# Performance work log

Measured on AMD Instinct MI355X. Metric: run time of the kernel, lower is better.

## Reference

```python
import jax, jax.numpy as jnp
import numpy as np

N = 32; AUD = 128; MO = 256; LXM = 128; L = 600; B = 20; BL = 30
AH = 256; AE = 256; HID = 1024; OUT = 256; DEPTH = 2
IN_DIM = MO + AE + LXM      # 640
GRU_IN = IN_DIM + HID       # 1664


def gelu(x):
    return jax.nn.gelu(x, approximate=False)


def conv1d(x, w, b, stride=1, pad=0):
    y = jax.lax.conv_general_dilated(x, w, (stride,), [(pad, pad)],
                                     dimension_numbers=('NCH', 'OIH', 'NCH'))
    return y + b[None, :, None]


def layernorm(x, g, b, eps=1e-5):
    mu = jnp.mean(x, -1, keepdims=True)
    var = jnp.mean((x - mu) ** 2, -1, keepdims=True)
    return (x - mu) * jax.lax.rsqrt(var + eps) * g + b


def gru_cell(x, h, wih, whh, bih, bhh):
    gi = x @ wih.T + bih
    gh = h @ whh.T + bhh
    ir, iz, inn = jnp.split(gi, 3, -1)
    hr, hz, hn = jnp.split(gh, 3, -1)
    r = jax.nn.sigmoid(ir + hr)
    z = jax.nn.sigmoid(iz + hz)
    n = jnp.tanh(inn + r * hn)
    return (1.0 - z) * n + z * h


def setup_inputs():
    key = jax.random.key(0)
    ks = jax.random.split(key, 32)
    rn = lambda i, sh: jax.random.normal(ks[i], sh, jnp.float32) * 0.02
    z = lambda d: jnp.zeros((d,), jnp.float32)
    return {
        'aud': jax.random.normal(ks[0], (N, AUD, L), jnp.float32),
        'mo': jax.random.normal(ks[1], (N, MO, L), jnp.float32),
        'lxm': jax.random.normal(ks[2], (N, LXM, B), jnp.float32),
        'ae_w0': rn(3, (AH, AUD, 7)), 'ae_b0': z(AH),
        'ae_w1': rn(4, (AH, AH, 5)), 'ae_b1': z(AH),
        'ae_w2': rn(5, (AE, AH, 4)), 'ae_b2': z(AE),
        'ae_w3': rn(6, (AE, AE)), 'ae_b3': z(AE),
        'ae_ln_g': jnp.ones((AE,), jnp.float32), 'ae_ln_b': z(AE),
        'ci_w0': rn(7, (HID, MO + LXM)), 'ci_b0': z(HID),
        'ci_w1': rn(8, (HID, HID)), 'ci_b1': z(HID),
        'ci_w2': rn(9, (HID * DEPTH, HID)), 'ci_b2': z(HID * DEPTH),
        'dec_in_w': rn(10, (HID, IN_DIM)), 'dec_in_b': z(HID),
        'gru_wih0': rn(11, (3 * HID, GRU_IN)), 'gru_whh0': rn(12, (3 * HID, HID)),
        'gru_bih0': z(3 * HID), 'gru_bhh0': z(3 * HID),
        'gru_wih1': rn(13, (3 * HID, HID)), 'gru_whh1': rn(14, (3 * HID, HID)),
        'gru_bih1': z(3 * HID), 'gru_bhh1': z(3 * HID),
        'dec_ln_g': jnp.ones((HID,), jnp.float32), 'dec_ln_b': z(HID),
        'pred_w': rn(15, (OUT, HID)), 'pred_b': z(OUT),
    }


def reference(aud, mo, lxm, ae_w0, ae_b0, ae_w1, ae_b1, ae_w2, ae_b2, ae_w3, ae_b3,
              ae_ln_g, ae_ln_b, ci_w0, ci_b0, ci_w1, ci_b1, ci_w2, ci_b2,
              dec_in_w, dec_in_b, gru_wih0, gru_whh0, gru_bih0, gru_bhh0,
              gru_wih1, gru_whh1, gru_bih1, gru_bhh1, dec_ln_g, dec_ln_b,
              pred_w, pred_b):
    Nb = B - 2
    # Overlapping 3*BL audio windows for all blocks, encoded in one batched pass.
    win = jnp.stack([aud[:, :, b * BL:(b + 3) * BL] for b in range(Nb)], 0)  # [Nb,N,AUD,3BL]
    x = win.reshape(Nb * N, AUD, 3 * BL)
    x = gelu(conv1d(x, ae_w0, ae_b0))
    x = gelu(conv1d(x, ae_w1, ae_b1))
    x = gelu(conv1d(x, ae_w2, ae_b2, stride=2, pad=1))
    x = jnp.transpose(x, (0, 2, 1))                  # NDL -> NLD
    x = gelu(x @ ae_w3.T + ae_b3)
    x = layernorm(x, ae_ln_g, ae_ln_b)
    # Only frames 0..BL-1 of each encoded window are consumed by the decode loop.
    aud_seq = jnp.transpose(x[:, :BL, :].reshape(Nb, N, BL, AE), (0, 2, 1, 3)).reshape(Nb * BL, N, AE)
    lxm_seq = jnp.repeat(jnp.transpose(lxm[:, :, 1:B - 1], (2, 0, 1)), BL, axis=0)  # [T,N,LXM]
    # Cell state initializer.
    ci = gelu(jnp.concatenate([mo[:, :, BL - 1], lxm[:, :, 0]], -1) @ ci_w0.T + ci_b0)
    ci = gelu(ci @ ci_w1.T + ci_b1)
    h0 = jnp.transpose((ci @ ci_w2.T + ci_b2).reshape(N, DEPTH, HID), (1, 0, 2))  # [DEPTH,N,HID]

    def step(carry, inputs):
        pre_mo, h = carry
        a_t, l_t = inputs
        xcat = jnp.concatenate([pre_mo, a_t, l_t], -1)
        emb = gelu(xcat @ dec_in_w.T + dec_in_b)
        gin = jnp.concatenate([emb, xcat], -1)
        h0n = gru_cell(gin, h[0], gru_wih0, gru_whh0, gru_bih0, gru_bhh0)
        h1n = gru_cell(h0n, h[1], gru_wih1, gru_whh1, gru_bih1, gru_bhh1)
        pred = layernorm(h1n, dec_ln_g, dec_ln_b) @ pred_w.T + pred_b
        return (pred, jnp.stack([h0n, h1n])), pred

    _, preds = jax.lax.scan(step, (mo[:, :, BL - 1], h0), (aud_seq, lxm_seq))
    return jnp.transpose(preds, (1, 2, 0))  # [N, OUT, (B-2)*BL]
```

## Files before the change

kernel.cpp:

```cpp
#include <hip/hip_runtime.h>


typedef unsigned short u16;
typedef __attribute__((ext_vector_type(8))) short short8;
typedef __attribute__((ext_vector_type(4))) float f32x4;

#define GELU_FLG 1
#define BF16_FLG 2
#define NBLK 213
#define DEC_STEPS 540

__device__ __forceinline__ u16 f2b(float f){
  union { float f; unsigned u; } c; c.f = f;
  return (u16)((c.u + 0x7fffu + ((c.u >> 16) & 1u)) >> 16);
}
__device__ __forceinline__ short8 ld8(const u16* p){
  return *reinterpret_cast<const short8*>(p);
}
__device__ __forceinline__ short8 lds8(const void* p){
  return *reinterpret_cast<const short8*>(p);
}
__device__ __forceinline__ float ldfc(const float* p){
  return __hip_atomic_load(p, __ATOMIC_RELAXED, __HIP_MEMORY_SCOPE_AGENT);
}
__device__ __forceinline__ void stfc(float* p, float v){
  __hip_atomic_store(p, v, __ATOMIC_RELAXED, __HIP_MEMORY_SCOPE_AGENT);
}
__device__ __forceinline__ void stu32c(void* p, unsigned v){
  __hip_atomic_store((unsigned*)p, v, __ATOMIC_RELAXED, __HIP_MEMORY_SCOPE_AGENT);
}
__device__ __forceinline__ void st16c(u16* p, unsigned v){
  asm volatile("global_store_short %0, %1, off sc0 sc1" :: "v"(p), "v"(v) : "memory");
}
__device__ __forceinline__ f32x4 mfma16(short8 a, short8 b, f32x4 c){
  return __builtin_amdgcn_mfma_f32_16x16x32_bf16(a, b, c, 0, 0, 0);
}
__device__ __forceinline__ float gelu_f(float x){
  return 0.5f * x * (1.f + erff(x * 0.70710678118654752f));
}
__device__ __forceinline__ float sigmoid_f(float x){
  return 1.f / (1.f + __expf(-x));
}
__device__ __forceinline__ float tanh_f(float x){
  float e = __expf(-2.f * x);
  return (1.f - e) / (1.f + e);
}

template<int KB>
__device__ __forceinline__ void stageN(unsigned* ldsbase, const void* gbase, int lane, int q){
  const char* g = (const char*)gbase;
  #pragma unroll
  for (int c = 0; c < KB / 4; ++c){
    int cc = q + c * 4;
    __builtin_amdgcn_global_load_lds((const unsigned*)(g + (size_t)cc * 1024 + lane * 16),
                                     ldsbase + cc * 256, 16, 0, 0);
  }
}


__global__ void f2b_k(const float* __restrict__ s, u16* __restrict__ d, int n){
  int i = blockIdx.x * 256 + threadIdx.x;
  if (i < n) d[i] = f2b(s[i]);
}

__global__ void gather_xc_k(const float* __restrict__ mo, const float* __restrict__ lxm,
                            u16* __restrict__ xc, u16* __restrict__ pre_mo){
  int i = blockIdx.x * 256 + threadIdx.x;
  if (i >= 32 * 384) return;
  int n = i / 384, c = i - n * 384;
  float v = (c < 256) ? mo[(size_t)(n * 256 + c) * 600 + 29]
                      : lxm[(size_t)(n * 128 + (c - 256)) * 20];
  u16 h = f2b(v);
  xc[i] = h;
  if (c < 256) pre_mo[n * 256 + c] = h;
}

__global__ void lxm_g_k(const float* __restrict__ lxm, u16* __restrict__ o){
  int i = blockIdx.x * 256 + threadIdx.x;
  if (i >= 18 * 32 * 128) return;
  int c = i & 127, rest = i >> 7;
  int n = rest & 31, b = rest >> 5;
  o[i] = f2b(lxm[(size_t)(n * 128 + c) * 20 + 1 + b]);
}

__global__ void split_h_k(const float* __restrict__ hraw, u16* __restrict__ h0, u16* __restrict__ h1,
                          float* __restrict__ h0f, float* __restrict__ h1f){
  int i = blockIdx.x * 256 + threadIdx.x;
  if (i >= 32 * 1024) return;
  int n = i >> 10, c = i & 1023;
  float a = hraw[(size_t)n * 2048 + c];
  float b = hraw[(size_t)n * 2048 + 1024 + c];
  h0[i] = f2b(a); h1[i] = f2b(b);
  h0f[i] = a;     h1f[i] = b;
}

__global__ void build_xc0_k(const u16* __restrict__ pre_mo, const u16* __restrict__ aud_seq,
                            const u16* __restrict__ lxm_b, u16* __restrict__ xc0){
  int i = blockIdx.x * 256 + threadIdx.x;
  if (i >= 32 * 640) return;
  int n = i / 640, c = i - n * 640;
  u16 v;
  if (c < 256) v = pre_mo[n * 256 + c];
  else if (c < 512) v = aud_seq[n * 256 + (c - 256)];
  else v = lxm_b[n * 128 + (c - 512)];
  xc0[i] = v;
}

__global__ void swz_emb_k(const u16* __restrict__ src, u16* __restrict__ dst){
  int i = blockIdx.x * 256 + threadIdx.x;
  if (i >= 32 * 1024) return;
  int row = i >> 10, col = i & 1023;
  unsigned boff = (unsigned)(row * 2048) + (((unsigned)col * 2) ^ ((row & 7) << 4));
  *(u16*)((char*)dst + boff) = src[i];
}

__global__ void t_wpT_k(const float* __restrict__ wp, u16* __restrict__ wpT){
  int i = blockIdx.x * 256 + threadIdx.x;
  if (i >= 1024 * 256) return;
  int h = i >> 8, j = i & 255;
  wpT[i] = f2b(wp[(size_t)j * 1024 + h]);
}

__global__ void foldW_k(const float* __restrict__ src, const float* __restrict__ g,
                        const float* __restrict__ b, const float* __restrict__ addb,
                        u16* __restrict__ Wg, float* __restrict__ S, float* __restrict__ B, int R){
  int row = blockIdx.x * 4 + (threadIdx.x >> 6);
  if (row >= R) return;
  int lane = threadIdx.x & 63;
  const float* sr = src + (size_t)row * 1024;
  float s = 0.f, bb = 0.f;
  #pragma unroll
  for (int k = 0; k < 16; ++k){
    int c = lane + k * 64;
    float w = sr[c], gw = w * g[c];
    Wg[(size_t)row * 1024 + c] = f2b(gw);
    s += gw; bb += w * b[c];
  }
  #pragma unroll
  for (int m = 1; m < 64; m <<= 1){ s += __shfl_xor(s, m); bb += __shfl_xor(bb, m); }
  if (lane == 0){ S[row] = s; B[row] = bb + (addb ? addb[row] : 0.f); }
}

__global__ void vfold_k(const float* __restrict__ W, int ldw, int off, const float* __restrict__ pb,
                        const float* __restrict__ base, float* __restrict__ v, int R){
  int row = blockIdx.x * 4 + (threadIdx.x >> 6);
  if (row >= R) return;
  int lane = threadIdx.x & 63;
  const float* wr = W + (size_t)row * ldw + off;
  float s = 0.f;
  #pragma unroll
  for (int k = 0; k < 4; ++k){ int j = lane + k * 64; s += wr[j] * pb[j]; }
  #pragma unroll
  for (int m = 1; m < 64; m <<= 1) s += __shfl_xor(s, m);
  if (lane == 0) v[row] = s + (base ? base[row] : 0.f);
}


__global__ void im2col0_k(const float* __restrict__ aud, u16* __restrict__ A, int row0, long long tot){
  long long i = (long long)blockIdx.x * 256 + threadIdx.x;
  if (i >= tot) return;
  int k = (int)(i % 896);
  int row = row0 + (int)(i / 896);
  int ci = k / 7, kk = k - ci * 7;
  int p = row % 84, bn = row / 84;
  int b = bn >> 5, n = bn & 31;
  A[i] = f2b(aud[(size_t)(n * 128 + ci) * 600 + b * 30 + p + kk]);
}

__global__ void im2col1_k(const u16* __restrict__ O0, u16* __restrict__ A, int row0, long long tot){
  long long i = (long long)blockIdx.x * 256 + threadIdx.x;
  if (i >= tot) return;
  int k = (int)(i % 1280);
  int row = row0 + (int)(i / 1280);
  int ci = k / 5, kk = k - ci * 5;
  int p = row % 80, bn = row / 80;
  A[i] = O0[(size_t)(bn * 84 + p + kk) * 256 + ci];
}

__global__ void im2col2_k(const u16* __restrict__ O1, u16* __restrict__ A, int row0, long long tot){
  long long i = (long long)blockIdx.x * 256 + threadIdx.x;
  if (i >= tot) return;
  int k = (int)(i & 1023);
  int row = row0 + (int)(i >> 10);
  int ci = k >> 2, kk = k & 3;
  int p = row % 40, bn = row / 40;
  int pos = 2 * p - 1 + kk;
  A[i] = (pos >= 0 && pos < 80) ? O1[(size_t)(bn * 80 + pos) * 256 + ci] : (u16)0;
}


__global__ void gemm_bt(const u16* __restrict__ A, int lda,
                        const u16* __restrict__ W, int ldw, const float* __restrict__ bias,
                        void* __restrict__ outp, int M, int N, int K, int flags){
  const int lane = threadIdx.x & 63, widx = threadIdx.x >> 6;
  const int m0 = blockIdx.x * 64 + widx * 16;
  if (m0 >= M) return;
  const int n0 = blockIdx.y * 64;
  const int r = lane & 15, g4 = lane >> 4;
  const u16* arow = A + (size_t)(m0 + r) * lda + g4 * 8;
  const u16* wrow = W + (size_t)(n0 + r) * ldw + g4 * 8;
  f32x4 acc[4];
  const f32x4 FZ = {0.f, 0.f, 0.f, 0.f};
  acc[0] = FZ; acc[1] = FZ; acc[2] = FZ; acc[3] = FZ;
  for (int k = 0; k < K; k += 32){
    short8 a = ld8(arow + k);
    #pragma unroll
    for (int j = 0; j < 4; ++j)
      acc[j] = mfma16(a, ld8(wrow + (size_t)j * 16 * ldw + k), acc[j]);
  }
  #pragma unroll
  for (int j = 0; j < 4; ++j){
    int col = n0 + j * 16 + r;
    float bv = bias ? bias[col] : 0.f;
    #pragma unroll
    for (int q = 0; q < 4; ++q){
      int row = m0 + g4 * 4 + q;
      float v = acc[j][q] + bv;
      if (flags & GELU_FLG) v = gelu_f(v);
      if (flags & BF16_FLG) ((u16*)outp)[(size_t)row * N + col] = f2b(v);
      else                  ((float*)outp)[(size_t)row * N + col] = v;
    }
  }
}


__global__ void enc_ln_k(const float* __restrict__ O3, const float* __restrict__ g,
                         const float* __restrict__ bb, u16* __restrict__ aud_seq){
  int rid = blockIdx.x * 4 + (threadIdx.x >> 6);
  int lane = threadIdx.x & 63;
  int b = rid / 960, rem = rid - b * 960;
  int p2 = rem >> 5, n = rem & 31;
  int orow = (b * 32 + n) * 40 + p2;
  const float4 v = *reinterpret_cast<const float4*>(O3 + (size_t)orow * 256 + lane * 4);
  float s  = v.x + v.y + v.z + v.w;
  float s2 = v.x * v.x + v.y * v.y + v.z * v.z + v.w * v.w;
  #pragma unroll
  for (int m = 1; m < 64; m <<= 1){ s += __shfl_xor(s, m); s2 += __shfl_xor(s2, m); }
  float mu = s * (1.f / 256.f);
  float var = s2 * (1.f / 256.f) - mu * mu;
  float rs = rsqrtf(var + 1e-5f);
  int c = lane * 4;
  u16* dst = aud_seq + (size_t)rid * 256 + c;
  dst[0] = f2b((v.x - mu) * rs * g[c + 0] + bb[c + 0]);
  dst[1] = f2b((v.y - mu) * rs * g[c + 1] + bb[c + 1]);
  dst[2] = f2b((v.z - mu) * rs * g[c + 2] + bb[c + 2]);
  dst[3] = f2b((v.w - mu) * rs * g[c + 3] + bb[c + 3]);
}


struct DecArgs {
  const u16 *aud_seq, *lxm_b;
  const u16 *wih0, *whh0, *wih1, *whh1, *wd;
  const u16 *wpg, *Wdpg, *Wgpg;
  const float *Sp, *Bp, *S1, *B1, *S2, *B2, *vX, *vG;
  const float *bih0, *bhh0, *bih1, *bhh1;
  const u16 *h0init, *h1init;
  u16 *embR, *h0R, *h1R;
  float *statsR;
  float *GxR, *XalR, *GalR;
  float *h0f, *h1f, *out;
  int *sync;
};

__device__ __forceinline__ void sigslot(int* slot, int ep){
  asm volatile("s_waitcnt vmcnt(0)" ::: "memory");
  __syncthreads();
  if (threadIdx.x == 0)
    __hip_atomic_store(slot, ep, __ATOMIC_RELAXED, __HIP_MEMORY_SCOPE_AGENT);
}
__device__ __forceinline__ void waitflag(const int* flag, int tgt){
  if (threadIdx.x == 0){
    while (__hip_atomic_load(flag, __ATOMIC_RELAXED, __HIP_MEMORY_SCOPE_AGENT) < tgt)
      __builtin_amdgcn_s_sleep(1);
  }
  __syncthreads();
}
__device__ __forceinline__ void stage_fence(){
  asm volatile("s_waitcnt vmcnt(0)" ::: "memory");
  __syncthreads();
}

__global__ __launch_bounds__(256, 1) void decode_k(DecArgs A){
  const int tid = threadIdx.x;
  const int lane = tid & 63, q = tid >> 6;
  const int r = lane & 15, g4 = lane >> 4;
  const int blk = blockIdx.x;
  __shared__ __align__(16) unsigned smw[25088];
  char* const stg = (char*)smw;
  float* const exch = (float*)(smw + 16384);
  float* const stgStats = (float*)(smw + 16384);
  const f32x4 FZ = {0.f, 0.f, 0.f, 0.f};
  const int sw = (r & 7) << 4;
  int* const slotH0 = A.sync;
  int* const slotH1 = A.sync + 128 * 16;
  int* const slotPE = A.sync + 256 * 16;
  int* const slotAL = A.sync + 384 * 16;
  int* const flagH0 = A.sync + 512 * 16;
  int* const flagH1 = A.sync + 768 * 16;
  int* const flagPE = A.sync + 1024 * 16;
  int* const flagAL = A.sync + 1280 * 16;

  if (blk < 64){
    const int c0 = blk * 16;
    const int kq = q * 256;
    int* const myFpe = flagPE + blk * 16;
    int* const myFh0 = flagH0 + blk * 16;
    int* const mySlot = slotH0 + blk * 16;
    short8 we[24], wh[24];
    #pragma unroll
    for (int g = 0; g < 3; ++g)
      #pragma unroll
      for (int ch = 0; ch < 8; ++ch){
        we[g * 8 + ch] = ld8(A.wih0 + (size_t)(g * 1024 + c0 + r) * 1664 + kq + ch * 32 + g4 * 8);
        wh[g * 8 + ch] = ld8(A.whh0 + (size_t)(g * 1024 + c0 + r) * 1024 + kq + ch * 32 + g4 * 8);
      }
    const int n_c = tid >> 3;
    const int cc0 = (tid & 7) * 2;
    const int colA = c0 + cc0, colB = colA + 1;
    const unsigned stoff = (unsigned)(n_c * 2048) + (((unsigned)colA * 2) ^ ((n_c & 7) << 4));
    const float bi_r[2] = {A.bih0[colA], A.bih0[colB]};
    const float bi_z[2] = {A.bih0[1024 + colA], A.bih0[1024 + colB]};
    const float bi_n[2] = {A.bih0[2048 + colA], A.bih0[2048 + colB]};
    const float bh_r[2] = {A.bhh0[colA], A.bhh0[colB]};
    const float bh_z[2] = {A.bhh0[1024 + colA], A.bhh0[1024 + colB]};
    const float bh_n[2] = {A.bhh0[2048 + colA], A.bhh0[2048 + colB]};
    f32x4 ar[2], az[2], ani[2], anh[2];
    ar[0] = FZ; ar[1] = FZ; az[0] = FZ; az[1] = FZ; ani[0] = FZ; ani[1] = FZ; anh[0] = FZ; anh[1] = FZ;
    #pragma unroll
    for (int ch = 0; ch < 8; ++ch){
      short8 a0 = ld8(A.h0init + r * 1024 + kq + ch * 32 + g4 * 8);
      short8 a1 = ld8(A.h0init + (16 + r) * 1024 + kq + ch * 32 + g4 * 8);
      ar[0] = mfma16(a0, wh[ch], ar[0]);        ar[1] = mfma16(a1, wh[ch], ar[1]);
      az[0] = mfma16(a0, wh[8 + ch], az[0]);    az[1] = mfma16(a1, wh[8 + ch], az[1]);
      anh[0] = mfma16(a0, wh[16 + ch], anh[0]); anh[1] = mfma16(a1, wh[16 + ch], anh[1]);
    }
    #pragma unroll 1
    for (int t = 0; t < DEC_STEPS; ++t){
      if (t > 0) waitflag(myFpe, t);
      const u16*  embT = A.embR + (size_t)t * 32768;
      u16*        h0T  = A.h0R  + (size_t)t * 32768;
      const float* GxT = A.GxR + (size_t)(t & 7) * 98304;
      stageN<64>(smw, embT, lane, q);
      float pgr[2], pgz[2], pgn[2], phf[2];
      #pragma unroll
      for (int e = 0; e < 2; ++e){
        int col = c0 + cc0 + e;
        pgr[e] = ldfc(GxT + n_c * 3072 + col);
        pgz[e] = ldfc(GxT + n_c * 3072 + 1024 + col);
        pgn[e] = ldfc(GxT + n_c * 3072 + 2048 + col);
        phf[e] = A.h0f[n_c * 1024 + col];
      }
      stage_fence();
      #pragma unroll
      for (int ch = 0; ch < 8; ++ch){
        int off = ((kq + ch * 32 + g4 * 8) * 2) ^ sw;
        short8 a0 = lds8(stg + r * 2048 + off);
        short8 a1 = lds8(stg + (16 + r) * 2048 + off);
        ar[0] = mfma16(a0, we[ch], ar[0]);        ar[1] = mfma16(a1, we[ch], ar[1]);
        az[0] = mfma16(a0, we[8 + ch], az[0]);    az[1] = mfma16(a1, we[8 + ch], az[1]);
        ani[0] = mfma16(a0, we[16 + ch], ani[0]); ani[1] = mfma16(a1, we[16 + ch], ani[1]);
      }
      #pragma unroll
      for (int m = 0; m < 2; ++m)
        #pragma unroll
        for (int j = 0; j < 4; ++j){
          int row = m * 16 + g4 * 4 + j;
          exch[((q * 4 + 0) * 32 + row) * 17 + r] = ar[m][j];
          exch[((q * 4 + 1) * 32 + row) * 17 + r] = az[m][j];
          exch[((q * 4 + 2) * 32 + row) * 17 + r] = ani[m][j];
          exch[((q * 4 + 3) * 32 + row) * 17 + r] = anh[m][j];
        }
      __syncthreads();
      float hv2[2];
      #pragma unroll
      for (int e = 0; e < 2; ++e){
        int cc = cc0 + e, col = c0 + cc;
        float sr = bi_r[e] + bh_r[e] + pgr[e];
        float sz = bi_z[e] + bh_z[e] + pgz[e];
        float si = bi_n[e] + pgn[e];
        float sh = bh_n[e];
        #pragma unroll
        for (int qq = 0; qq < 4; ++qq){
          sr += exch[((qq * 4 + 0) * 32 + n_c) * 17 + cc];
          sz += exch[((qq * 4 + 1) * 32 + n_c) * 17 + cc];
          si += exch[((qq * 4 + 2) * 32 + n_c) * 17 + cc];
          sh += exch[((qq * 4 + 3) * 32 + n_c) * 17 + cc];
        }
        float rg = sigmoid_f(sr), zg = sigmoid_f(sz);
        float ng = tanh_f(si + rg * sh);
        float hv = (1.f - zg) * ng + zg * phf[e];
        A.h0f[n_c * 1024 + col] = hv;
        hv2[e] = hv;
      }
      stu32c((char*)h0T + stoff,
             (unsigned)f2b(hv2[0]) | ((unsigned)f2b(hv2[1]) << 16));
      __syncthreads();
      sigslot(mySlot, t + 1);
      waitflag(myFh0, t + 1);
      stageN<64>(smw, h0T, lane, q);
      stage_fence();
      ar[0] = FZ; ar[1] = FZ; az[0] = FZ; az[1] = FZ; ani[0] = FZ; ani[1] = FZ; anh[0] = FZ; anh[1] = FZ;
      #pragma unroll
      for (int ch = 0; ch < 8; ++ch){
        int off = ((kq + ch * 32 + g4 * 8) * 2) ^ sw;
        short8 a0 = lds8(stg + r * 2048 + off);
        short8 a1 = lds8(stg + (16 + r) * 2048 + off);
        ar[0] = mfma16(a0, wh[ch], ar[0]);        ar[1] = mfma16(a1, wh[ch], ar[1]);
        az[0] = mfma16(a0, wh[8 + ch], az[0]);    az[1] = mfma16(a1, wh[8 + ch], az[1]);
        anh[0] = mfma16(a0, wh[16 + ch], anh[0]); anh[1] = mfma16(a1, wh[16 + ch], anh[1]);
      }
    }
  } else if (blk < 128){
    const int c0 = (blk - 64) * 16;
    const int kq = q * 256;
    int* const myFh0 = flagH0 + blk * 16;
    int* const myFh1 = flagH1 + blk * 16;
    int* const mySlot = slotH1 + (blk - 64) * 16;
    short8 wi[24], wh[24];
    #pragma unroll
    for (int g = 0; g < 3; ++g)
      #pragma unroll
      for (int ch = 0; ch < 8; ++ch){
        wi[g * 8 + ch] = ld8(A.wih1 + (size_t)(g * 1024 + c0 + r) * 1024 + kq + ch * 32 + g4 * 8);
        wh[g * 8 + ch] = ld8(A.whh1 + (size_t)(g * 1024 + c0 + r) * 1024 + kq + ch * 32 + g4 * 8);
      }
    const int n_c = tid >> 3;
    const int cc0 = (tid & 7) * 2;
    const int colA = c0 + cc0, colB = colA + 1;
    const unsigned stoff = (unsigned)(n_c * 2048) + (((unsigned)colA * 2) ^ ((n_c & 7) << 4));
    const float bi_r[2] = {A.bih1[colA], A.bih1[colB]};
    const float bi_z[2] = {A.bih1[1024 + colA], A.bih1[1024 + colB]};
    const float bi_n[2] = {A.bih1[2048 + colA], A.bih1[2048 + colB]};
    const float bh_r[2] = {A.bhh1[colA], A.bhh1[colB]};
    const float bh_z[2] = {A.bhh1[1024 + colA], A.bhh1[1024 + colB]};
    const float bh_n[2] = {A.bhh1[2048 + colA], A.bhh1[2048 + colB]};
    f32x4 ar[2], az[2], ani[2], anh[2];
    ar[0] = FZ; ar[1] = FZ; az[0] = FZ; az[1] = FZ; ani[0] = FZ; ani[1] = FZ; anh[0] = FZ; anh[1] = FZ;
    #pragma unroll
    for (int ch = 0; ch < 8; ++ch){
      short8 a0 = ld8(A.h1init + r * 1024 + kq + ch * 32 + g4 * 8);
      short8 a1 = ld8(A.h1init + (16 + r) * 1024 + kq + ch * 32 + g4 * 8);
      ar[0] = mfma16(a0, wh[ch], ar[0]);        ar[1] = mfma16(a1, wh[ch], ar[1]);
      az[0] = mfma16(a0, wh[8 + ch], az[0]);    az[1] = mfma16(a1, wh[8 + ch], az[1]);
      anh[0] = mfma16(a0, wh[16 + ch], anh[0]); anh[1] = mfma16(a1, wh[16 + ch], anh[1]);
    }
    #pragma unroll 1
    for (int t = 0; t < DEC_STEPS; ++t){
      waitflag(myFh0, t + 1);
      const u16* h0T = A.h0R + (size_t)t * 32768;
      u16*       h1T = A.h1R + (size_t)t * 32768;
      stageN<64>(smw, h0T, lane, q);
      float phf[2];
      phf[0] = A.h1f[n_c * 1024 + colA];
      phf[1] = A.h1f[n_c * 1024 + colB];
      stage_fence();
      #pragma unroll
      for (int ch = 0; ch < 8; ++ch){
        int off = ((kq + ch * 32 + g4 * 8) * 2) ^ sw;
        short8 a0 = lds8(stg + r * 2048 + off);
        short8 a1 = lds8(stg + (16 + r) * 2048 + off);
        ar[0] = mfma16(a0, wi[ch], ar[0]);        ar[1] = mfma16(a1, wi[ch], ar[1]);
        az[0] = mfma16(a0, wi[8 + ch], az[0]);    az[1] = mfma16(a1, wi[8 + ch], az[1]);
        ani[0] = mfma16(a0, wi[16 + ch], ani[0]); ani[1] = mfma16(a1, wi[16 + ch], ani[1]);
      }
      #pragma unroll
      for (int m = 0; m < 2; ++m)
        #pragma unroll
        for (int j = 0; j < 4; ++j){
          int row = m * 16 + g4 * 4 + j;
          exch[((q * 4 + 0) * 32 + row) * 17 + r] = ar[m][j];
          exch[((q * 4 + 1) * 32 + row) * 17 + r] = az[m][j];
          exch[((q * 4 + 2) * 32 + row) * 17 + r] = ani[m][j];
          exch[((q * 4 + 3) * 32 + row) * 17 + r] = anh[m][j];
        }
      __syncthreads();
      float hv2[2];
      #pragma unroll
      for (int e = 0; e < 2; ++e){
        int cc = cc0 + e, col = c0 + cc;
        float sr = bi_r[e] + bh_r[e];
        float sz = bi_z[e] + bh_z[e];
        float si = bi_n[e];
        float sh = bh_n[e];
        #pragma unroll
        for (int qq = 0; qq < 4; ++qq){
          sr += exch[((qq * 4 + 0) * 32 + n_c) * 17 + cc];
          sz += exch[((qq * 4 + 1) * 32 + n_c) * 17 + cc];
          si += exch[((qq * 4 + 2) * 32 + n_c) * 17 + cc];
          sh += exch[((qq * 4 + 3) * 32 + n_c) * 17 + cc];
        }
        float rg = sigmoid_f(sr), zg = sigmoid_f(sz);
        float ng = tanh_f(si + rg * sh);
        float hv = (1.f - zg) * ng + zg * phf[e];
        A.h1f[n_c * 1024 + col] = hv;
        hv2[e] = hv;
      }
      stu32c((char*)h1T + stoff,
             (unsigned)f2b(hv2[0]) | ((unsigned)f2b(hv2[1]) << 16));
      float sv = hv2[0] + hv2[1], sq = hv2[0] * hv2[0] + hv2[1] * hv2[1];
      sv += __shfl_xor(sv, 1); sq += __shfl_xor(sq, 1);
      sv += __shfl_xor(sv, 2); sq += __shfl_xor(sq, 2);
      sv += __shfl_xor(sv, 4); sq += __shfl_xor(sq, 4);
      if ((tid & 7) == 0){
        stfc(A.statsR + (size_t)t * 4096 + (blk - 64) * 64 + n_c, sv);
        stfc(A.statsR + (size_t)t * 4096 + (blk - 64) * 64 + 32 + n_c, sq);
      }
      __syncthreads();
      sigslot(mySlot, t + 1);
      waitflag(myFh1, t + 1);
      stageN<64>(smw, h1T, lane, q);
      stage_fence();
      ar[0] = FZ; ar[1] = FZ; az[0] = FZ; az[1] = FZ; ani[0] = FZ; ani[1] = FZ; anh[0] = FZ; anh[1] = FZ;
      #pragma unroll
      for (int ch = 0; ch < 8; ++ch){
        int off = ((kq + ch * 32 + g4 * 8) * 2) ^ sw;
        short8 a0 = lds8(stg + r * 2048 + off);
        short8 a1 = lds8(stg + (16 + r) * 2048 + off);
        ar[0] = mfma16(a0, wh[ch], ar[0]);        ar[1] = mfma16(a1, wh[ch], ar[1]);
        az[0] = mfma16(a0, wh[8 + ch], az[0]);    az[1] = mfma16(a1, wh[8 + ch], az[1]);
        anh[0] = mfma16(a0, wh[16 + ch], anh[0]); anh[1] = mfma16(a1, wh[16 + ch], anh[1]);
      }
    }
  } else if (blk < 196){
    const int tile = (blk - 128) * 4 + q;
    int* const myFh1 = flagH1 + blk * 16;
    int* const myFal = flagAL + blk * 16;
    int* const mySlot = slotPE + (blk - 128) * 16;
    int jt, c0;
    const u16* wsrc; const float *Sv, *Bv;
    if (tile < 16)      { jt = 0; c0 = tile * 16;        wsrc = A.wpg;  Sv = A.Sp; Bv = A.Bp; }
    else if (tile < 80) { jt = 1; c0 = (tile - 16) * 16; wsrc = A.Wdpg; Sv = A.S1; Bv = A.B1; }
    else                { jt = 2; c0 = (tile - 80) * 16; wsrc = A.Wgpg; Sv = A.S2; Bv = A.B2; }
    short8 w[32];
    #pragma unroll
    for (int ch = 0; ch < 32; ++ch)
      w[ch] = ld8(wsrc + (size_t)(c0 + r) * 1024 + ch * 32 + g4 * 8);
    const float Sc = Sv[c0 + r], Bc = Bv[c0 + r];
    const int col = c0 + r;
    #pragma unroll 1
    for (int t = 0; t < DEC_STEPS; ++t){
      waitflag(myFh1, t + 1);
      waitflag(myFal, t + 1);
      const u16*   h1T = A.h1R + (size_t)t * 32768;
      const float* stT = A.statsR + (size_t)t * 4096;
      const int sl = (t + 1) & 7;
      stageN<64>(smw, h1T, lane, q);
      stageN<16>(smw + 16384, stT, lane, q);
      const float* XalT = A.XalR + (size_t)sl * 32768;
      const float* GalT = A.GalR + (size_t)sl * 98304;
      float addv[2][4];
      #pragma unroll
      for (int m = 0; m < 2; ++m)
        #pragma unroll
        for (int j = 0; j < 4; ++j){
          int n = m * 16 + g4 * 4 + j;
          addv[m][j] = (jt == 1) ? ldfc(XalT + n * 1024 + col)
                     : (jt == 2) ? ldfc(GalT + n * 3072 + col) : 0.f;
        }
      stage_fence();
      float sacc = 0.f;
      #pragma unroll
      for (int b2 = 0; b2 < 64; ++b2) sacc += stgStats[b2 * 64 + lane];
      float muA[2][4], rsA[2][4];
      #pragma unroll
      for (int m = 0; m < 2; ++m)
        #pragma unroll
        for (int j = 0; j < 4; ++j){
          int n = m * 16 + g4 * 4 + j;
          float sv = __shfl(sacc, n), sq = __shfl(sacc, 32 + n);
          float mu = sv * (1.f / 1024.f);
          muA[m][j] = mu;
          rsA[m][j] = rsqrtf(sq * (1.f / 1024.f) - mu * mu + 1e-5f);
        }
      f32x4 a0 = FZ, a1 = FZ;
      #pragma unroll
      for (int ch = 0; ch < 32; ++ch){
        int off = ((ch * 32 + g4 * 8) * 2) ^ sw;
        short8 x0 = lds8(stg + r * 2048 + off);
        short8 x1 = lds8(stg + (16 + r) * 2048 + off);
        a0 = mfma16(x0, w[ch], a0);
        a1 = mfma16(x1, w[ch], a1);
      }
      u16*   embN = A.embR + (size_t)(t + 1) * 32768;
      float* GxN  = A.GxR + (size_t)sl * 98304;
      #pragma unroll
      for (int m = 0; m < 2; ++m)
        #pragma unroll
        for (int j = 0; j < 4; ++j){
          int n = m * 16 + g4 * 4 + j;
          float acc = (m ? a1[j] : a0[j]);
          float v = rsA[m][j] * (acc - muA[m][j] * Sc) + Bc;
          if (jt == 0){
            A.out[(size_t)n * (256 * 540) + (size_t)col * 540 + t] = v;
          } else if (jt == 1){
            float pre = v + addv[m][j];
            unsigned boff = (unsigned)(n * 2048) + (((unsigned)col * 2) ^ ((n & 7) << 4));
            st16c((u16*)((char*)embN + boff), (unsigned)f2b(gelu_f(pre)));
          } else {
            stfc(GxN + n * 3072 + col, v + addv[m][j]);
          }
        }
      sigslot(mySlot, t + 1);
    }
  } else if (blk < 212){
    const int wg = (blk - 196) * 4 + q;
    int* const myFpe = flagPE + blk * 16;
    int* const mySlot = slotAL + (blk - 196) * 16;
    const int at0 = wg * 4;
    short8 w[48];
    float vb[4];
    #pragma unroll
    for (int j = 0; j < 4; ++j){
      int at = at0 + j;
      if (at < 64){
        #pragma unroll
        for (int ch = 0; ch < 12; ++ch)
          w[j * 12 + ch] = ld8(A.wd + (size_t)(at * 16 + r) * 640 + 256 + ch * 32 + g4 * 8);
        vb[j] = A.vX[at * 16 + r];
      } else {
        #pragma unroll
        for (int ch = 0; ch < 12; ++ch)
          w[j * 12 + ch] = ld8(A.wih0 + (size_t)((at - 64) * 16 + r) * 1664 + 1280 + ch * 32 + g4 * 8);
        vb[j] = A.vG[(at - 64) * 16 + r];
      }
    }
    #pragma unroll 1
    for (int t = 0; t < DEC_STEPS; ++t){
      if (t >= 8) waitflag(myFpe, t - 7);
      const int tn = t + 1;
      const int tread = (tn > 539) ? 539 : tn;
      const int bn = tread / 30;
      const int sl = tn & 7;
      float* XalW = A.XalR + (size_t)sl * 32768;
      float* GalW = A.GalR + (size_t)sl * 98304;
      short8 af0[12], af1[12];
      #pragma unroll
      for (int ch = 0; ch < 12; ++ch){
        int kk = ch * 32 + g4 * 8;
        if (ch < 8){
          af0[ch] = ld8(A.aud_seq + ((size_t)tread * 32 + r) * 256 + kk);
          af1[ch] = ld8(A.aud_seq + ((size_t)tread * 32 + 16 + r) * 256 + kk);
        } else {
          af0[ch] = ld8(A.lxm_b + ((size_t)bn * 32 + r) * 128 + kk - 256);
          af1[ch] = ld8(A.lxm_b + ((size_t)bn * 32 + 16 + r) * 128 + kk - 256);
        }
      }
      #pragma unroll
      for (int j = 0; j < 4; ++j){
        f32x4 c0a = FZ, c1a = FZ;
        #pragma unroll
        for (int ch = 0; ch < 12; ++ch){
          c0a = mfma16(af0[ch], w[j * 12 + ch], c0a);
          c1a = mfma16(af1[ch], w[j * 12 + ch], c1a);
        }
        int at = at0 + j;
        #pragma unroll
        for (int m = 0; m < 2; ++m)
          #pragma unroll
          for (int jj = 0; jj < 4; ++jj){
            int n = m * 16 + g4 * 4 + jj;
            float v = (m ? c1a[jj] : c0a[jj]) + vb[j];
            if (at < 64) stfc(XalW + n * 1024 + at * 16 + r, v);
            else         stfc(GalW + n * 3072 + (at - 64) * 16 + r, v);
          }
      }
      sigslot(mySlot, tn);
    }
  } else {
    const int NPs[4] = {64, 64, 68, 16};
    const int NP = NPs[q];
    int* const slotG = A.sync + q * 128 * 16;
    int* const flagG = A.sync + (512 + q * 256) * 16;
    const int idx1 = (lane < NP) ? lane : 0;
    const int extra = NP - 64;
    #pragma unroll 1
    for (int t = 1; t <= DEC_STEPS; ++t){
      for (;;){
        int v = __hip_atomic_load(slotG + idx1 * 16, __ATOMIC_RELAXED, __HIP_MEMORY_SCOPE_AGENT);
        bool ok = (v >= t);
        if (extra > 0 && lane < extra){
          int v2 = __hip_atomic_load(slotG + (64 + lane) * 16, __ATOMIC_RELAXED, __HIP_MEMORY_SCOPE_AGENT);
          ok = ok && (v2 >= t);
        }
        if (__all(ok)) break;
        __builtin_amdgcn_s_sleep(1);
      }
      #pragma unroll 1
      for (int c = lane; c < NBLK; c += 64)
        __hip_atomic_store(flagG + c * 16, t, __ATOMIC_RELAXED, __HIP_MEMORY_SCOPE_AGENT);
    }
  }
}


extern "C" void kernel_launch(void* const* d_in, const int* in_sizes, int n_in,
                              void* d_out, int out_size, void* d_ws, size_t ws_size,
                              hipStream_t stream) {
  enum { I_AUD=0, I_MO=1, I_LXM=2, I_AEW0=3, I_AEB0=4, I_AEW1=5, I_AEB1=6, I_AEW2=7, I_AEB2=8,
         I_AEW3=9, I_AEB3=10, I_AELNG=11, I_AELNB=12, I_CIW0=13, I_CIB0=14, I_CIW1=15, I_CIB1=16,
         I_CIW2=17, I_CIB2=18, I_DECW=19, I_DECB=20, I_WIH0=21, I_WHH0=22, I_BIH0=23, I_BHH0=24,
         I_WIH1=25, I_WHH1=26, I_BIH1=27, I_BHH1=28, I_LNG=29, I_LNB=30, I_PREDW=31, I_PREDB=32 };

  char* base = (char*)d_ws;
  size_t off = 0;
  auto alloc = [&](size_t bytes)->void*{
    void* p = base + off;
    off += (bytes + 255) & ~(size_t)255;
    return p;
  };

  u16* wd_b   = (u16*)alloc((size_t)1024*640*2);
  u16* wih0_b = (u16*)alloc((size_t)3072*1664*2);
  u16* whh0_b = (u16*)alloc((size_t)3072*1024*2);
  u16* wih1_b = (u16*)alloc((size_t)3072*1024*2);
  u16* whh1_b = (u16*)alloc((size_t)3072*1024*2);
  u16* wc0    = (u16*)alloc((size_t)1024*384*2);
  u16* wc1    = (u16*)alloc((size_t)1024*1024*2);
  u16* wc2    = (u16*)alloc((size_t)2048*1024*2);
  u16* w0k    = (u16*)alloc((size_t)256*896*2);
  u16* w1k    = (u16*)alloc((size_t)256*1280*2);
  u16* w2k    = (u16*)alloc((size_t)256*1024*2);
  u16* w3k    = (u16*)alloc((size_t)256*256*2);
  u16* wpT    = (u16*)alloc((size_t)1024*256*2);
  u16* wpg    = (u16*)alloc((size_t)256*1024*2);
  u16* Wdpg   = (u16*)alloc((size_t)1024*1024*2);
  u16* Wgpg   = (u16*)alloc((size_t)3072*1024*2);
  float* Sp = (float*)alloc(256*4);   float* Bp = (float*)alloc(256*4);
  float* S1 = (float*)alloc(1024*4);  float* B1 = (float*)alloc(1024*4);
  float* S2 = (float*)alloc(3072*4);  float* B2 = (float*)alloc(3072*4);
  float* vX = (float*)alloc(1024*4);  float* vG = (float*)alloc(3072*4);
  u16* aud_seq = (u16*)alloc((size_t)540*32*256*2);
  u16* lxm_b   = (u16*)alloc((size_t)18*32*128*2);
  u16* xc      = (u16*)alloc((size_t)32*384*2);
  u16* xc0     = (u16*)alloc((size_t)32*640*2);
  u16* ci1     = (u16*)alloc((size_t)32*1024*2);
  u16* ci2     = (u16*)alloc((size_t)32*1024*2);
  float* hraw  = (float*)alloc((size_t)32*2048*4);
  u16* h0i     = (u16*)alloc((size_t)32*1024*2);
  u16* h1i     = (u16*)alloc((size_t)32*1024*2);
  float* h0f   = (float*)alloc((size_t)32*1024*4);
  float* h1f   = (float*)alloc((size_t)32*1024*4);
  u16* pre_mo  = (u16*)alloc((size_t)32*256*2);
  u16* emb0    = (u16*)alloc((size_t)32*1024*2);
  float* GxR   = (float*)alloc((size_t)8*32*3072*4);
  float* XalR  = (float*)alloc((size_t)8*32*1024*4);
  float* GalR  = (float*)alloc((size_t)8*32*3072*4);
  int* syncb   = (int*)alloc((size_t)1536*16*4);
  char* enc_base = base + off;
  u16* O0   = (u16*)alloc((size_t)48384*256*2);
  u16* O1   = (u16*)alloc((size_t)46080*256*2);
  u16* O2   = (u16*)alloc((size_t)23040*256*2);
  float* O3 = (float*)alloc((size_t)23040*256*4);
  u16* Abuf = (u16*)alloc((size_t)23040*1280*2);
  float* Wdp_f = (float*)Abuf;
  float* Wgp_f = (float*)((char*)Abuf + (size_t)1024*1024*4 + 256);
  u16* embR     = (u16*)enc_base;
  u16* h0R      = embR + (size_t)541*32768;
  u16* h1R      = h0R + (size_t)540*32768;
  float* statsR = (float*)(h1R + (size_t)540*32768);
  (void)ws_size; (void)in_sizes; (void)n_in; (void)out_size;

  const float* aud = (const float*)d_in[I_AUD];
  const float* mo  = (const float*)d_in[I_MO];
  const float* lxm = (const float*)d_in[I_LXM];
  float* out = (float*)d_out;

  auto cdiv = [](long long a, long long b)->int{ return (int)((a + b - 1) / b); };
  auto cvt = [&](int idx, u16* dst, int n){
    f2b_k<<<cdiv(n,256), 256, 0, stream>>>((const float*)d_in[idx], dst, n);
  };

  cvt(I_DECW, wd_b,   1024*640);
  cvt(I_WIH0, wih0_b, 3072*1664);
  cvt(I_WHH0, whh0_b, 3072*1024);
  cvt(I_WIH1, wih1_b, 3072*1024);
  cvt(I_WHH1, whh1_b, 3072*1024);
  cvt(I_CIW0, wc0,    1024*384);
  cvt(I_CIW1, wc1,    1024*1024);
  cvt(I_CIW2, wc2,    2048*1024);
  cvt(I_AEW0, w0k,    256*896);
  cvt(I_AEW1, w1k,    256*1280);
  cvt(I_AEW2, w2k,    256*1024);
  cvt(I_AEW3, w3k,    256*256);

  for (int c = 0; c < 2; ++c){
    int row0 = c * 24192;
    long long tot = (long long)24192 * 896;
    im2col0_k<<<cdiv(tot,256), 256, 0, stream>>>(aud, Abuf, row0, tot);
    gemm_bt<<<dim3(24192/64, 4), 256, 0, stream>>>(Abuf, 896, w0k, 896, (const float*)d_in[I_AEB0],
        O0 + (size_t)row0*256, 24192, 256, 896, GELU_FLG|BF16_FLG);
  }
  for (int c = 0; c < 2; ++c){
    int row0 = c * 23040;
    long long tot = (long long)23040 * 1280;
    im2col1_k<<<cdiv(tot,256), 256, 0, stream>>>(O0, Abuf, row0, tot);
    gemm_bt<<<dim3(23040/64, 4), 256, 0, stream>>>(Abuf, 1280, w1k, 1280, (const float*)d_in[I_AEB1],
        O1 + (size_t)row0*256, 23040, 256, 1280, GELU_FLG|BF16_FLG);
  }
  {
    long long tot = (long long)23040 * 1024;
    im2col2_k<<<cdiv(tot,256), 256, 0, stream>>>(O1, Abuf, 0, tot);
    gemm_bt<<<dim3(23040/64, 4), 256, 0, stream>>>(Abuf, 1024, w2k, 1024, (const float*)d_in[I_AEB2],
        O2, 23040, 256, 1024, GELU_FLG|BF16_FLG);
  }
  gemm_bt<<<dim3(23040/64, 4), 256, 0, stream>>>(O2, 256, w3k, 256, (const float*)d_in[I_AEB3],
      O3, 23040, 256, 256, GELU_FLG);
  enc_ln_k<<<4320, 256, 0, stream>>>(O3, (const float*)d_in[I_AELNG], (const float*)d_in[I_AELNB], aud_seq);

  lxm_g_k<<<cdiv(18*32*128,256), 256, 0, stream>>>(lxm, lxm_b);
  gather_xc_k<<<cdiv(32*384,256), 256, 0, stream>>>(mo, lxm, xc, pre_mo);
  gemm_bt<<<dim3(1,16), 256, 0, stream>>>(xc, 384, wc0, 384, (const float*)d_in[I_CIB0],
      ci1, 32, 1024, 384, GELU_FLG|BF16_FLG);
  gemm_bt<<<dim3(1,16), 256, 0, stream>>>(ci1, 1024, wc1, 1024, (const float*)d_in[I_CIB1],
      ci2, 32, 1024, 1024, GELU_FLG|BF16_FLG);
  gemm_bt<<<dim3(1,32), 256, 0, stream>>>(ci2, 1024, wc2, 1024, (const float*)d_in[I_CIB2],
      hraw, 32, 2048, 1024, 0);
  split_h_k<<<cdiv(32*1024,256), 256, 0, stream>>>(hraw, h0i, h1i, h0f, h1f);

  t_wpT_k<<<cdiv(1024*256,256), 256, 0, stream>>>((const float*)d_in[I_PREDW], wpT);
  gemm_bt<<<dim3(16,16), 256, 0, stream>>>(wd_b, 640, wpT, 256, nullptr, Wdp_f, 1024, 1024, 256, 0);
  gemm_bt<<<dim3(48,16), 256, 0, stream>>>(wih0_b + 1024, 1664, wpT, 256, nullptr, Wgp_f, 3072, 1024, 256, 0);
  foldW_k<<<cdiv(1024,4), 256, 0, stream>>>(Wdp_f, (const float*)d_in[I_LNG], (const float*)d_in[I_LNB],
      nullptr, Wdpg, S1, B1, 1024);
  foldW_k<<<cdiv(3072,4), 256, 0, stream>>>(Wgp_f, (const float*)d_in[I_LNG], (const float*)d_in[I_LNB],
      nullptr, Wgpg, S2, B2, 3072);
  foldW_k<<<cdiv(256,4), 256, 0, stream>>>((const float*)d_in[I_PREDW], (const float*)d_in[I_LNG],
      (const float*)d_in[I_LNB], (const float*)d_in[I_PREDB], wpg, Sp, Bp, 256);
  vfold_k<<<cdiv(1024,4), 256, 0, stream>>>((const float*)d_in[I_DECW], 640, 0,
      (const float*)d_in[I_PREDB], (const float*)d_in[I_DECB], vX, 1024);
  vfold_k<<<cdiv(3072,4), 256, 0, stream>>>((const float*)d_in[I_WIH0], 1664, 1024,
      (const float*)d_in[I_PREDB], nullptr, vG, 3072);

  build_xc0_k<<<cdiv(32*640,256), 256, 0, stream>>>(pre_mo, aud_seq, lxm_b, xc0);
  gemm_bt<<<dim3(1,16), 256, 0, stream>>>(xc0, 640, wd_b, 640, (const float*)d_in[I_DECB],
      emb0, 32, 1024, 640, GELU_FLG|BF16_FLG);
  swz_emb_k<<<cdiv(32*1024,256), 256, 0, stream>>>(emb0, embR);
  gemm_bt<<<dim3(1,48), 256, 0, stream>>>(xc0, 640, wih0_b + 1024, 1664, nullptr,
      GxR, 32, 3072, 640, 0);

  hipMemsetAsync(syncb, 0, (size_t)1536*16*4, stream);

  DecArgs da;
  da.aud_seq = aud_seq; da.lxm_b = lxm_b;
  da.wih0 = wih0_b; da.whh0 = whh0_b; da.wih1 = wih1_b; da.whh1 = whh1_b; da.wd = wd_b;
  da.wpg = wpg; da.Wdpg = Wdpg; da.Wgpg = Wgpg;
  da.Sp = Sp; da.Bp = Bp; da.S1 = S1; da.B1 = B1; da.S2 = S2; da.B2 = B2; da.vX = vX; da.vG = vG;
  da.bih0 = (const float*)d_in[I_BIH0]; da.bhh0 = (const float*)d_in[I_BHH0];
  da.bih1 = (const float*)d_in[I_BIH1]; da.bhh1 = (const float*)d_in[I_BHH1];
  da.h0init = h0i; da.h1init = h1i;
  da.embR = embR; da.h0R = h0R; da.h1R = h1R; da.statsR = statsR;
  da.GxR = GxR; da.XalR = XalR; da.GalR = GalR;
  da.h0f = h0f; da.h1f = h1f;
  da.out = out; da.sync = syncb;
  decode_k<<<dim3(NBLK), dim3(256), 0, stream>>>(da);
}
```

Measured before the change: 8.684 ms.

## Replace aggregator-block flag broadcast with direct per-block slot polling

Removes the dedicated sync-aggregator block, which watched group slots and rebroadcast per-block flags. Each consumer block now polls the producer slots of its group directly with one wavefront and a wave-wide all-vote. This drops one hop of latency from every inter-stage handoff across the 540 decode steps. In exchange, many blocks now poll the same slot cache lines at once, which raises memory traffic contention.

```diff
diff --git a/kernel.cpp b/kernel.cpp
--- a/kernel.cpp
+++ b/kernel.cpp
@@ -7,7 +7,7 @@
 
 #define GELU_FLG 1
 #define BF16_FLG 2
-#define NBLK 213
+#define NBLK 212
 #define DEC_STEPS 540
 
 __device__ __forceinline__ u16 f2b(float f){
@@ -268,10 +268,19 @@
   if (threadIdx.x == 0)
     __hip_atomic_store(slot, ep, __ATOMIC_RELAXED, __HIP_MEMORY_SCOPE_AGENT);
 }
-__device__ __forceinline__ void waitflag(const int* flag, int tgt){
-  if (threadIdx.x == 0){
-    while (__hip_atomic_load(flag, __ATOMIC_RELAXED, __HIP_MEMORY_SCOPE_AGENT) < tgt)
+__device__ __forceinline__ void wait_grp(const int* slotG, int nx, const int* slotE, int tgt){
+  if (threadIdx.x < 64){
+    const int lane = threadIdx.x;
+    for (;;){
+      int v = __hip_atomic_load(slotG + lane * 16, __ATOMIC_RELAXED, __HIP_MEMORY_SCOPE_AGENT);
+      bool ok = (v >= tgt);
+      if (lane < nx){
+        int v2 = __hip_atomic_load(slotE + lane * 16, __ATOMIC_RELAXED, __HIP_MEMORY_SCOPE_AGENT);
+        ok = ok && (v2 >= tgt);
+      }
+      if (__all(ok)) break;
       __builtin_amdgcn_s_sleep(1);
+    }
   }
   __syncthreads();
 }
@@ -295,16 +304,10 @@
   int* const slotH1 = A.sync + 128 * 16;
   int* const slotPE = A.sync + 256 * 16;
   int* const slotAL = A.sync + 384 * 16;
-  int* const flagH0 = A.sync + 512 * 16;
-  int* const flagH1 = A.sync + 768 * 16;
-  int* const flagPE = A.sync + 1024 * 16;
-  int* const flagAL = A.sync + 1280 * 16;
 
   if (blk < 64){
     const int c0 = blk * 16;
     const int kq = q * 256;
-    int* const myFpe = flagPE + blk * 16;
-    int* const myFh0 = flagH0 + blk * 16;
     int* const mySlot = slotH0 + blk * 16;
     short8 we[24], wh[24];
     #pragma unroll
@@ -336,7 +339,7 @@
     }
     #pragma unroll 1
     for (int t = 0; t < DEC_STEPS; ++t){
-      if (t > 0) waitflag(myFpe, t);
+      if (t > 0) wait_grp(slotPE, 4, slotPE + 64 * 16, t);
       const u16*  embT = A.embR + (size_t)t * 32768;
       u16*        h0T  = A.h0R  + (size_t)t * 32768;
       const float* GxT = A.GxR + (size_t)(t & 7) * 98304;
@@ -396,7 +399,7 @@
              (unsigned)f2b(hv2[0]) | ((unsigned)f2b(hv2[1]) << 16));
       __syncthreads();
       sigslot(mySlot, t + 1);
-      waitflag(myFh0, t + 1);
+      wait_grp(slotH0, 0, slotH0, t + 1);
       stageN<64>(smw, h0T, lane, q);
       stage_fence();
       ar[0] = FZ; ar[1] = FZ; az[0] = FZ; az[1] = FZ; ani[0] = FZ; ani[1] = FZ; anh[0] = FZ; anh[1] = FZ;
@@ -413,8 +416,6 @@
   } else if (blk < 128){
     const int c0 = (blk - 64) * 16;
     const int kq = q * 256;
-    int* const myFh0 = flagH0 + blk * 16;
-    int* const myFh1 = flagH1 + blk * 16;
     int* const mySlot = slotH1 + (blk - 64) * 16;
     short8 wi[24], wh[24];
     #pragma unroll
@@ -446,7 +447,7 @@
     }
     #pragma unroll 1
     for (int t = 0; t < DEC_STEPS; ++t){
-      waitflag(myFh0, t + 1);
+      wait_grp(slotH0, 0, slotH0, t + 1);
       const u16* h0T = A.h0R + (size_t)t * 32768;
       u16*       h1T = A.h1R + (size_t)t * 32768;
       stageN<64>(smw, h0T, lane, q);
@@ -507,7 +508,7 @@
       }
       __syncthreads();
       sigslot(mySlot, t + 1);
-      waitflag(myFh1, t + 1);
+      wait_grp(slotH1, 0, slotH1, t + 1);
       stageN<64>(smw, h1T, lane, q);
       stage_fence();
       ar[0] = FZ; ar[1] = FZ; az[0] = FZ; az[1] = FZ; ani[0] = FZ; ani[1] = FZ; anh[0] = FZ; anh[1] = FZ;
@@ -523,8 +524,6 @@
     }
   } else if (blk < 196){
     const int tile = (blk - 128) * 4 + q;
-    int* const myFh1 = flagH1 + blk * 16;
-    int* const myFal = flagAL + blk * 16;
     int* const mySlot = slotPE + (blk - 128) * 16;
     int jt, c0;
     const u16* wsrc; const float *Sv, *Bv;
@@ -539,8 +538,7 @@
     const int col = c0 + r;
     #pragma unroll 1
     for (int t = 0; t < DEC_STEPS; ++t){
-      waitflag(myFh1, t + 1);
-      waitflag(myFal, t + 1);
+      wait_grp(slotH1, 16, slotAL, t + 1);
       const u16*   h1T = A.h1R + (size_t)t * 32768;
       const float* stT = A.statsR + (size_t)t * 4096;
       const int sl = (t + 1) & 7;
@@ -602,9 +600,8 @@
         }
       sigslot(mySlot, t + 1);
     }
-  } else if (blk < 212){
+  } else {
     const int wg = (blk - 196) * 4 + q;
-    int* const myFpe = flagPE + blk * 16;
     int* const mySlot = slotAL + (blk - 196) * 16;
     const int at0 = wg * 4;
     short8 w[48];
@@ -626,7 +623,7 @@
     }
     #pragma unroll 1
     for (int t = 0; t < DEC_STEPS; ++t){
-      if (t >= 8) waitflag(myFpe, t - 7);
+      if (t >= 8) wait_grp(slotPE, 4, slotPE + 64 * 16, t - 7);
       const int tn = t + 1;
       const int tread = (tn > 539) ? 539 : tn;
       const int bn = tread / 30;
@@ -665,29 +662,6 @@
           }
       }
       sigslot(mySlot, tn);
-    }
-  } else {
-    const int NPs[4] = {64, 64, 68, 16};
-    const int NP = NPs[q];
-    int* const slotG = A.sync + q * 128 * 16;
-    int* const flagG = A.sync + (512 + q * 256) * 16;
-    const int idx1 = (lane < NP) ? lane : 0;
-    const int extra = NP - 64;
-    #pragma unroll 1
-    for (int t = 1; t <= DEC_STEPS; ++t){
-      for (;;){
-        int v = __hip_atomic_load(slotG + idx1 * 16, __ATOMIC_RELAXED, __HIP_MEMORY_SCOPE_AGENT);
-        bool ok = (v >= t);
-        if (extra > 0 && lane < extra){
-          int v2 = __hip_atomic_load(slotG + (64 + lane) * 16, __ATOMIC_RELAXED, __HIP_MEMORY_SCOPE_AGENT);
-          ok = ok && (v2 >= t);
-        }
-        if (__all(ok)) break;
-        __builtin_amdgcn_s_sleep(1);
-      }
-      #pragma unroll 1
-      for (int c = lane; c < NBLK; c += 64)
-        __hip_atomic_store(flagG + c * 16, t, __ATOMIC_RELAXED, __HIP_MEMORY_SCOPE_AGENT);
     }
   }
 }
@@ -745,7 +719,7 @@
   float* GxR   = (float*)alloc((size_t)8*32*3072*4);
   float* XalR  = (float*)alloc((size_t)8*32*1024*4);
   float* GalR  = (float*)alloc((size_t)8*32*3072*4);
-  int* syncb   = (int*)alloc((size_t)1536*16*4);
+  int* syncb   = (int*)alloc((size_t)512*16*4);
   char* enc_base = base + off;
   u16* O0   = (u16*)alloc((size_t)48384*256*2);
   u16* O1   = (u16*)alloc((size_t)46080*256*2);
@@ -838,7 +812,7 @@
   gemm_bt<<<dim3(1,48), 256, 0, stream>>>(xc0, 640, wih0_b + 1024, 1664, nullptr,
       GxR, 32, 3072, 640, 0);
 
-  hipMemsetAsync(syncb, 0, (size_t)1536*16*4, stream);
+  hipMemsetAsync(syncb, 0, (size_t)512*16*4, stream);
 
   DecArgs da;
   da.aud_seq = aud_seq; da.lxm_b = lxm_b;
```

After: 8.078 ms. 1.08x faster.
